# Kernel optimization log

Hardware: AMD Instinct MI355X
Metric: run time of the kernel (lower is better)

## Reference

```python
import jax, jax.numpy as jnp
import numpy as np

B, N, M, D, H, DH, DFF, L = 64, 2048, 32, 128, 4, 32, 512, 2
EPS = 1e-5


def setup_inputs() -> dict:
    key = jax.random.key(0)
    ks = jax.random.split(key, 8)
    def xav(k, shape, fan_in):
        return jax.random.normal(k, shape, jnp.float32) * (1.0 / np.sqrt(fan_in))
    return {
        "feat": jax.random.normal(ks[0], (B, N, D), jnp.float32),
        "I_pts": xav(ks[1], (L, M, D), D),                # inducing points per ISAB layer
        "Wq": xav(ks[2], (L, 2, D, H * DH), D),
        "Wk": xav(ks[3], (L, 2, D, H * DH), D),
        "Wv": xav(ks[4], (L, 2, D, H * DH), D),
        "Wo": xav(ks[5], (L, 2, H * DH, D), H * DH),
        "W1": xav(ks[6], (L, 2, D, DFF), D),
        "b1": jnp.zeros((L, 2, DFF), jnp.float32),
        "W2": xav(ks[7], (L, 2, DFF, D), DFF),
        "b2": jnp.zeros((L, 2, D), jnp.float32),
        "ln1_g": jnp.ones((L, 2, D), jnp.float32),
        "ln1_b": jnp.zeros((L, 2, D), jnp.float32),
        "ln2_g": jnp.ones((L, 2, D), jnp.float32),
        "ln2_b": jnp.zeros((L, 2, D), jnp.float32),
    }


def _layer_norm(x, g, b):
    mu = jnp.mean(x, axis=-1, keepdims=True)
    var = jnp.mean(jnp.square(x - mu), axis=-1, keepdims=True)
    return (x - mu) * jax.lax.rsqrt(var + EPS) * g + b


def _mha(q_feat, kv_feat, Wq, Wk, Wv, Wo, W1, b1, W2, b2, g1, be1, g2, be2):
    # q_feat: [B, nq, D], kv_feat: [B, nk, D]
    nq, nk = q_feat.shape[1], kv_feat.shape[1]
    Q = (q_feat @ Wq).reshape(B, nq, H, DH)
    K = (kv_feat @ Wk).reshape(B, nk, H, DH)
    V = (kv_feat @ Wv).reshape(B, nk, H, DH)
    # edge score = sum_d(q*k)/sqrt(d_head); edge_softmax normalizes over kv per query
    scores = jnp.einsum('bqhd,bkhd->bhqk', Q, K) / np.sqrt(DH)
    att = jax.nn.softmax(scores, axis=-1)
    out = jnp.einsum('bhqk,bkhd->bqhd', att, V).reshape(B, nq, H * DH)
    sa = out @ Wo
    x = _layer_norm(q_feat + sa, g1, be1)
    ffn = jax.nn.relu(x @ W1 + b1) @ W2 + b2
    return _layer_norm(x + ffn, g2, be2)


def reference(feat, I_pts, Wq, Wk, Wv, Wo, W1, b1, W2, b2, ln1_g, ln1_b, ln2_g, ln2_b):
    x = feat
    for l in range(L):  # ISAB layers
        query = jnp.broadcast_to(I_pts[l], (B, M, D))
        kv = x
        for j in range(2):  # induced -> set, then set -> induced
            rst = _mha(query, kv,
                       Wq[l, j], Wk[l, j], Wv[l, j], Wo[l, j],
                       W1[l, j], b1[l, j], W2[l, j], b2[l, j],
                       ln1_g[l, j], ln1_b[l, j], ln2_g[l, j], ln2_b[l, j])
            query, kv = kv, rst
        x = rst
    return x
```

## Files before the change

kernel.cpp:

```cpp
#include <hip/hip_runtime.h>
#include <hip/hip_bf16.h>

#define BB 64
#define NN 2048
#define MM 32
#define DD 128
#define HH 4
#define LL 2
#define BN (BB*NN)
#define BM (BB*MM)

typedef short bf16x8 __attribute__((ext_vector_type(8)));
typedef float f32x4 __attribute__((ext_vector_type(4)));
#define MFMA __builtin_amdgcn_mfma_f32_16x16x32_bf16

__device__ __forceinline__ unsigned short f2bf(float f){
  union { float f; unsigned int u; } v; v.f = f;
  unsigned int r = 0x7FFFu + ((v.u >> 16) & 1u);
  return (unsigned short)((v.u + r) >> 16);
}
__device__ __forceinline__ float bf2f(short u){
  union { unsigned int u; float f; } v; v.u = ((unsigned int)(unsigned short)u) << 16; return v.f;
}
__device__ __forceinline__ float ldf(const float* p){ return *p; }
__device__ __forceinline__ float ldf(const unsigned short* p){ return bf2f((short)*p); }
__device__ __forceinline__ void stf(float* p, float v){ *p = v; }
__device__ __forceinline__ void stf(unsigned short* p, float v){ *p = f2bf(v); }

__device__ __forceinline__ bf16x8 cvt8(const float* __restrict__ p){
  float4 a = *reinterpret_cast<const float4*>(p);
  float4 b = *reinterpret_cast<const float4*>(p + 4);
  bf16x8 r;
  r[0]=(short)f2bf(a.x); r[1]=(short)f2bf(a.y); r[2]=(short)f2bf(a.z); r[3]=(short)f2bf(a.w);
  r[4]=(short)f2bf(b.x); r[5]=(short)f2bf(b.y); r[6]=(short)f2bf(b.z); r[7]=(short)f2bf(b.w);
  return r;
}

template<int NW>
__device__ __forceinline__ void stage_img(const unsigned short* __restrict__ img,
                                          unsigned short* Wt){
  int wave = threadIdx.x >> 6, lane = threadIdx.x & 63;
  #pragma unroll
  for (int i = 0; i < 32/NW; i++){
    int off = ((i*NW + wave) << 9);
    const unsigned short* gp = img + off + lane*8;
    unsigned short* lp = Wt + off;
    __builtin_amdgcn_global_load_lds(
        (__attribute__((address_space(1))) void*)gp,
        (__attribute__((address_space(3))) void*)lp, 16, 0, 0);
  }
}

__device__ __forceinline__ bf16x8 bfrag(const unsigned short* Wt, int cb, int k0, int lane){
  int c = (cb << 4) + (lane & 15);
  int kk = (k0 + ((lane >> 4) << 3)) ^ ((c & 7) << 3);
  return *reinterpret_cast<const bf16x8*>(Wt + (c << 7) + kk);
}

__device__ __forceinline__ void load_afrag(const float* __restrict__ A, int r0, int lane,
                                           bf16x8 af[2][4]){
  int li = lane & 15, lg = lane >> 4;
  #pragma unroll
  for (int s = 0; s < 2; s++){
    const float* ap = A + (size_t)(r0 + s*16 + li) * 128 + (lg << 3);
    #pragma unroll
    for (int ks = 0; ks < 4; ks++) af[s][ks] = cvt8(ap + ks*32);
  }
}
__device__ __forceinline__ void load_afrag(const unsigned short* __restrict__ A, int r0,
                                           int lane, bf16x8 af[2][4]){
  int li = lane & 15, lg = lane >> 4;
  #pragma unroll
  for (int s = 0; s < 2; s++){
    const unsigned short* ap = A + (size_t)(r0 + s*16 + li) * 128 + (lg << 3);
    #pragma unroll
    for (int ks = 0; ks < 4; ks++) af[s][ks] = *reinterpret_cast<const bf16x8*>(ap + ks*32);
  }
}

__device__ __forceinline__ void mfma_tile32(const bf16x8 af[2][4], const unsigned short* Wt,
                                            int lane, f32x4 acc[2][8]){
  #pragma unroll
  for (int ks = 0; ks < 4; ks++){
    #pragma unroll
    for (int cb = 0; cb < 8; cb++){
      bf16x8 b = bfrag(Wt, cb, ks*32, lane);
      acc[0][cb] = MFMA(af[0][ks], b, acc[0][cb], 0, 0, 0);
      acc[1][cb] = MFMA(af[1][ks], b, acc[1][cb], 0, 0, 0);
    }
  }
}

__device__ __forceinline__ void zero_acc(f32x4 acc[2][8]){
  #pragma unroll
  for (int s = 0; s < 2; s++)
    #pragma unroll
    for (int cb = 0; cb < 8; cb++) acc[s][cb] = (f32x4){0.f,0.f,0.f,0.f};
}

__device__ __forceinline__ void store_f32(const f32x4 acc[2][8], float* __restrict__ C,
                                          int r0, int lane){
  int li = lane & 15, lg = lane >> 4;
  #pragma unroll
  for (int s = 0; s < 2; s++)
    #pragma unroll
    for (int q = 0; q < 4; q++){
      float* crow = C + (size_t)(r0 + s*16 + lg*4 + q) * 128;
      #pragma unroll
      for (int cb = 0; cb < 8; cb++) crow[cb*16 + li] = acc[s][cb][q];
    }
}
__device__ __forceinline__ void store_bf16(const f32x4 acc[2][8], unsigned short* __restrict__ C,
                                           int r0, int lane){
  int li = lane & 15, lg = lane >> 4;
  #pragma unroll
  for (int s = 0; s < 2; s++)
    #pragma unroll
    for (int q = 0; q < 4; q++){
      unsigned short* crow = C + (size_t)(r0 + s*16 + lg*4 + q) * 128;
      #pragma unroll
      for (int cb = 0; cb < 8; cb++) crow[cb*16 + li] = f2bf(acc[s][cb][q]);
    }
}
__device__ __forceinline__ void store_st2(const f32x4 acc[2][8], float* __restrict__ St2,
                                          int b, int jb, int lane){
  int li = lane & 15, lg = lane >> 4;
  #pragma unroll
  for (int s = 0; s < 2; s++)
    #pragma unroll
    for (int cb = 0; cb < 8; cb++){
      float* p = St2 + ((size_t)(b*128 + cb*16 + li))*2048 + jb + s*16 + lg*4;
      *reinterpret_cast<f32x4*>(p) = acc[s][cb];
    }
}

template<typename RT, typename OT>
__device__ __forceinline__ void ln_ep(const f32x4 acc[8], const float* __restrict__ bias,
    const RT* __restrict__ resid, unsigned int resmask,
    const float* __restrict__ g, const float* __restrict__ beta,
    OT* __restrict__ C, int r0, int lane){
  int li = lane & 15, lg = lane >> 4;
  float gv[8], bv[8], biasv[8];
  #pragma unroll
  for (int cb = 0; cb < 8; cb++){
    int col = cb*16 + li;
    gv[cb] = g[col]; bv[cb] = beta[col];
    biasv[cb] = bias ? bias[col] : 0.f;
  }
  #pragma unroll
  for (int q = 0; q < 4; q++){
    int r = r0 + lg*4 + q;
    const RT* rrow = resid + (size_t)(r & resmask) * 128;
    float v[8], sum = 0.f, ss = 0.f;
    #pragma unroll
    for (int cb = 0; cb < 8; cb++){
      float x = acc[cb][q] + biasv[cb] + ldf(rrow + cb*16 + li);
      v[cb] = x; sum += x; ss += x*x;
    }
    #pragma unroll
    for (int mk = 1; mk < 16; mk <<= 1){ sum += __shfl_xor(sum, mk); ss += __shfl_xor(ss, mk); }
    float mu = sum * (1.f/128.f);
    float var = ss * (1.f/128.f) - mu*mu;
    float rs = rsqrtf(var + 1e-5f);
    OT* crow = C + (size_t)r * 128;
    #pragma unroll
    for (int cb = 0; cb < 8; cb++)
      stf(crow + cb*16 + li, (v[cb] - mu) * rs * gv[cb] + bv[cb]);
  }
}


__global__ __launch_bounds__(256) void prep_imgs(const float* __restrict__ Wq,
    const float* __restrict__ Wk, const float* __restrict__ Wv, const float* __restrict__ Wo,
    const float* __restrict__ W1, const float* __restrict__ W2, unsigned short* __restrict__ imgs){
  int slot = blockIdx.x;
  const float* src; int ldw;
  if (slot < 16){
    int j = slot >> 2, m = slot & 3;
    const float* base = (m==0) ? Wq : (m==1) ? Wk : (m==2) ? Wv : Wo;
    src = base + j*16384; ldw = 128;
  } else if (slot < 32){
    int s = slot - 16; int j = s >> 2, dc = s & 3;
    src = W1 + j*65536 + dc*128; ldw = 512;
  } else {
    int s = slot - 32; int j = s >> 2, dc = s & 3;
    src = W2 + j*65536 + dc*16384; ldw = 128;
  }
  unsigned short* img = imgs + (size_t)slot * 16384;
  for (int i = threadIdx.x; i < 16384; i += 256){
    int k = i >> 7, c = i & 127;
    img[(c << 7) + (k ^ ((c & 7) << 3))] = f2bf(src[k*ldw + c]);
  }
}

__global__ __launch_bounds__(256) void prep_phaseA(const float* __restrict__ I,
    const float* __restrict__ Wq, const float* __restrict__ Wk, unsigned short* __restrict__ WfImg){
  __shared__ float Qi[32*128];
  for (int i = threadIdx.x; i < 4096; i += 256){
    int q = i >> 7, c = i & 127;
    float s = 0.f;
    #pragma unroll 8
    for (int d = 0; d < 128; d++) s += I[q*128 + d] * Wq[d*128 + c];
    Qi[i] = s;
  }
  __syncthreads();
  const float scale = 0.17677669529663687f;
  for (int i = threadIdx.x; i < 1024; i += 256){
    int k = (blockIdx.x << 3) + (i >> 7), c = i & 127;
    int hc = c >> 5, qc = c & 31;
    float s = 0.f;
    #pragma unroll
    for (int d = 0; d < 32; d++) s += Wk[k*128 + hc*32 + d] * Qi[qc*128 + hc*32 + d];
    WfImg[(c << 7) + (k ^ ((c & 7) << 3))] = f2bf(s * scale);
  }
}

__global__ __launch_bounds__(256) void prep_phaseB(const float* __restrict__ Wq,
    const float* __restrict__ Wo, const float* __restrict__ Khb, const float* __restrict__ Vhb,
    unsigned short* __restrict__ WfImgs, unsigned short* __restrict__ GvImgs){
  __shared__ float Ks[32*129];
  __shared__ float Vs[32*129];
  __shared__ float Wqt[128*33];
  __shared__ float Wot[128*17];
  int b = blockIdx.x >> 3, part = blockIdx.x & 7;
  int hwf = part >> 1;
  for (int i = threadIdx.x; i < 4096; i += 256){
    int k = i >> 7, c = i & 127;
    Ks[k*129 + c] = Khb[b*4096 + i];
    Vs[k*129 + c] = Vhb[b*4096 + i];
  }
  for (int i = threadIdx.x; i < 4096; i += 256){
    int ci = i >> 5, d = i & 31;
    Wqt[ci*33 + d] = Wq[ci*128 + hwf*32 + d];
  }
  for (int i = threadIdx.x; i < 2048; i += 256){
    int row = i >> 4, cl = i & 15;
    Wot[row*17 + cl] = Wo[row*128 + part*16 + cl];
  }
  __syncthreads();
  const float scale = 0.17677669529663687f;
  unsigned short* wf = WfImgs + (size_t)b*16384;
  unsigned short* gv = GvImgs + (size_t)b*16384;
  {
    int ci = threadIdx.x & 127;
    float wq[32];
    #pragma unroll
    for (int d = 0; d < 32; d++) wq[d] = Wqt[ci*33 + d];
    #pragma unroll
    for (int it = 0; it < 8; it++){
      int kp = part*16 + (threadIdx.x >> 7) + it*2;
      int k = kp & 31;
      float s = 0.f;
      #pragma unroll
      for (int d = 0; d < 32; d++) s += wq[d] * Ks[k*129 + hwf*32 + d];
      wf[(kp << 7) + (ci ^ ((kp & 7) << 3))] = f2bf(s * scale);
    }
  }
  {
    int kp = threadIdx.x & 127;
    int h = kp >> 5, k = kp & 31;
    float vv[32];
    #pragma unroll
    for (int d = 0; d < 32; d++) vv[d] = Vs[k*129 + h*32 + d];
    #pragma unroll
    for (int it = 0; it < 8; it++){
      int c = part*16 + (threadIdx.x >> 7) + it*2;
      int cl = c & 15;
      float s = 0.f;
      #pragma unroll
      for (int d = 0; d < 32; d++) s += vv[d] * Wot[(h*32 + d)*17 + cl];
      gv[(c << 7) + (kp ^ ((c & 7) << 3))] = f2bf(s);
    }
  }
}

__global__ __launch_bounds__(512) void gemm_dual(const float* __restrict__ X,
    const unsigned short* __restrict__ img0, const unsigned short* __restrict__ img1,
    float* __restrict__ St2, unsigned short* __restrict__ Vb){
  __shared__ __align__(16) unsigned short W0[16384];
  __shared__ __align__(16) unsigned short W1s[16384];
  stage_img<8>(img0, W0);
  stage_img<8>(img1, W1s);
  __syncthreads();
  int lane = threadIdx.x & 63, wave = threadIdx.x >> 6;
  int r0 = blockIdx.x*256 + wave*32;
  int b = r0 >> 11, jb = r0 & 2047;
  bf16x8 af[2][4];
  load_afrag(X, r0, lane, af);
  f32x4 acc[2][8];
  zero_acc(acc);
  mfma_tile32(af, W0, lane, acc);
  store_st2(acc, St2, b, jb, lane);
  zero_acc(acc);
  mfma_tile32(af, W1s, lane, acc);
  store_bf16(acc, Vb, r0, lane);
}

__global__ __launch_bounds__(256) void gemm_img(const float* __restrict__ A,
    const unsigned short* __restrict__ img, float* __restrict__ C){
  __shared__ __align__(16) unsigned short Wt[16384];
  stage_img<4>(img, Wt);
  __syncthreads();
  int lane = threadIdx.x & 63, wave = threadIdx.x >> 6;
  int r0 = blockIdx.x*128 + wave*32;
  bf16x8 af[2][4];
  load_afrag(A, r0, lane, af);
  f32x4 acc[2][8];
  zero_acc(acc);
  mfma_tile32(af, Wt, lane, acc);
  store_f32(acc, C, r0, lane);
}

__global__ __launch_bounds__(256) void gemm_ln_f32A(const float* __restrict__ A,
    const unsigned short* __restrict__ img, const float* __restrict__ resid, unsigned int resmask,
    const float* __restrict__ g, const float* __restrict__ beta, float* __restrict__ C){
  __shared__ __align__(16) unsigned short Wt[16384];
  stage_img<4>(img, Wt);
  __syncthreads();
  int lane = threadIdx.x & 63, wave = threadIdx.x >> 6;
  int r0 = blockIdx.x*128 + wave*32;
  bf16x8 af[2][4];
  load_afrag(A, r0, lane, af);
  f32x4 acc[2][8];
  zero_acc(acc);
  mfma_tile32(af, Wt, lane, acc);
  ln_ep(acc[0], nullptr, resid, resmask, g, beta, C, r0,      lane);
  ln_ep(acc[1], nullptr, resid, resmask, g, beta, C, r0 + 16, lane);
}

__global__ __launch_bounds__(512) void attn_pv(const float* __restrict__ St2,
    const unsigned short* __restrict__ V, float* __restrict__ O){
  __shared__ __align__(16) unsigned short Vt[2][4096];
  __shared__ __align__(16) float Ocomb[4][64][4];
  __shared__ float scomb[4][16];
  int b = blockIdx.x >> 2, h = blockIdx.x & 3;
  int lane = threadIdx.x & 63, w = threadIdx.x >> 6;
  int li = lane & 15, lg = lane >> 4;
  int qh = w & 1, dh = (w >> 1) & 1, jh = w >> 2;
  int tq = w & 3;
  const float* Sp = St2 + ((size_t)(b*128 + h*32 + qh*16 + li)) * 2048 + jh*1024;
  const unsigned short* Vb = V + (size_t)b*NN*128 + h*32;
  unsigned short* VtJ = Vt[jh];
  int vrow = tq*32 + (lane >> 2);
  int vd0  = (lane & 3) * 8;
  const unsigned short* vsrc = Vb + ((size_t)(jh*1024 + vrow))*128 + vd0;

  f32x4 acc = (f32x4){0.f,0.f,0.f,0.f};
  float s = 0.f;
  f32x4 Ar[2][4][2];
  bf16x8 vr[2][2];

  #pragma unroll
  for (int t = 0; t < 2; t++)
    vr[0][t] = *reinterpret_cast<const bf16x8*>(vsrc + (size_t)t*16*128);
  #pragma unroll
  for (int ks = 0; ks < 4; ks++){
    Ar[0][ks][0] = *reinterpret_cast<const f32x4*>(Sp + ks*32 + lg*8);
    Ar[0][ks][1] = *reinterpret_cast<const f32x4*>(Sp + ks*32 + lg*8 + 4);
  }

  #pragma unroll
  for (int c = 0; c < 8; c++){
    const int cur = c & 1, nxt = cur ^ 1;
    __syncthreads();
    #pragma unroll
    for (int t = 0; t < 2; t++){
      int jl = vrow + t*16;
      #pragma unroll
      for (int e = 0; e < 8; e++){
        int d = vd0 + e;
        VtJ[(d << 7) + (jl ^ ((d & 7) << 3))] = (unsigned short)vr[cur][t][e];
      }
    }
    __syncthreads();
    if (c < 7){
      #pragma unroll
      for (int t = 0; t < 2; t++)
        vr[nxt][t] = *reinterpret_cast<const bf16x8*>(vsrc + ((size_t)(c+1)*128 + t*16)*128);
      #pragma unroll
      for (int ks = 0; ks < 4; ks++){
        Ar[nxt][ks][0] = *reinterpret_cast<const f32x4*>(Sp + (c+1)*128 + ks*32 + lg*8);
        Ar[nxt][ks][1] = *reinterpret_cast<const f32x4*>(Sp + (c+1)*128 + ks*32 + lg*8 + 4);
      }
    }
    #pragma unroll
    for (int ks = 0; ks < 4; ks++){
      bf16x8 a;
      #pragma unroll
      for (int i = 0; i < 4; i++){
        float pv = __expf(fminf(Ar[cur][ks][0][i], 60.f));
        s += pv; a[i] = (short)f2bf(pv);
      }
      #pragma unroll
      for (int i = 0; i < 4; i++){
        float pv = __expf(fminf(Ar[cur][ks][1][i], 60.f));
        s += pv; a[4+i] = (short)f2bf(pv);
      }
      bf16x8 bb = bfrag(VtJ, dh, ks*32, lane);
      acc = MFMA(a, bb, acc, 0, 0, 0);
    }
  }
  s += __shfl_xor(s, 16);
  s += __shfl_xor(s, 32);
  if (jh == 1){
    *reinterpret_cast<f32x4*>(&Ocomb[tq][lane][0]) = acc;
    if (lg == 0) scomb[tq][li] = s;
  }
  __syncthreads();
  if (jh == 0){
    acc += *reinterpret_cast<const f32x4*>(&Ocomb[tq][lane][0]);
    float inv = 1.f / (s + scomb[tq][li]);
    float* op = O + ((size_t)(b*MM + qh*16))*128 + h*32 + dh*16 + li;
    #pragma unroll
    for (int r = 0; r < 4; r++){
      float iv = __shfl(inv, lg*4 + r);
      op[(size_t)(lg*4 + r)*128] = acc[r] * iv;
    }
  }
}

__global__ __launch_bounds__(512) void attn_fused(const float* __restrict__ X,
    const unsigned short* __restrict__ WfImgs, const unsigned short* __restrict__ GvImgs,
    const float* __restrict__ g, const float* __restrict__ beta,
    unsigned short* __restrict__ X1){
  extern __shared__ __align__(16) unsigned short sm[];
  unsigned short* ht  = sm;
  unsigned short* WtF = sm + 32768;
  unsigned short* WtG = sm + 49152;
  int b = blockIdx.x >> 3;
  stage_img<8>(WfImgs + (size_t)b*16384, WtF);
  stage_img<8>(GvImgs + (size_t)b*16384, WtG);
  int lane = threadIdx.x & 63, wave = threadIdx.x >> 6;
  int li = lane & 15, lg = lane >> 4;
  int r0 = blockIdx.x*256 + wave*32;
  bf16x8 af[2][4];
  load_afrag(X, r0, lane, af);
  f32x4 acc[2][8];
  zero_acc(acc);
  __syncthreads();
  mfma_tile32(af, WtF, lane, acc);
  #pragma unroll
  for (int s = 0; s < 2; s++){
    #pragma unroll
    for (int q = 0; q < 4; q++){
      int rl = wave*32 + s*16 + lg*4 + q;
      #pragma unroll
      for (int h = 0; h < 4; h++){
        float v0 = acc[s][2*h][q], v1 = acc[s][2*h+1][q];
        float m = fmaxf(v0, v1);
        #pragma unroll
        for (int mk = 1; mk < 16; mk <<= 1) m = fmaxf(m, __shfl_xor(m, mk));
        float p0 = __expf(v0 - m), p1 = __expf(v1 - m);
        float ss = p0 + p1;
        #pragma unroll
        for (int mk = 1; mk < 16; mk <<= 1) ss += __shfl_xor(ss, mk);
        float inv = 1.f / ss;
        int c0 = h*32 + li, c1 = h*32 + 16 + li;
        ht[(rl << 7) + (c0 ^ ((rl & 7) << 3))] = f2bf(p0 * inv);
        ht[(rl << 7) + (c1 ^ ((rl & 7) << 3))] = f2bf(p1 * inv);
      }
    }
  }
  __syncthreads();
  zero_acc(acc);
  #pragma unroll
  for (int ks = 0; ks < 4; ks++){
    bf16x8 a[2];
    #pragma unroll
    for (int s = 0; s < 2; s++){
      int rl = wave*32 + s*16 + li;
      int kk = (ks*32 + (lg << 3)) ^ ((rl & 7) << 3);
      a[s] = *reinterpret_cast<const bf16x8*>(ht + (rl << 7) + kk);
    }
    #pragma unroll
    for (int cb = 0; cb < 8; cb++){
      bf16x8 bb = bfrag(WtG, cb, ks*32, lane);
      acc[0][cb] = MFMA(a[0], bb, acc[0][cb], 0, 0, 0);
      acc[1][cb] = MFMA(a[1], bb, acc[1][cb], 0, 0, 0);
    }
  }
  ln_ep(acc[0], nullptr, X, 0xFFFFFFFFu, g, beta, X1, r0,      lane);
  ln_ep(acc[1], nullptr, X, 0xFFFFFFFFu, g, beta, X1, r0 + 16, lane);
}

template<typename TA>
__global__ __launch_bounds__(512) void ffn_big(const TA* __restrict__ X,
    const unsigned short* __restrict__ W1i, const float* __restrict__ b1,
    const unsigned short* __restrict__ W2i, const float* __restrict__ b2,
    const float* __restrict__ g, const float* __restrict__ beta,
    float* __restrict__ OUT){
  extern __shared__ __align__(16) unsigned short sm[];
  unsigned short* ht  = sm;
  unsigned short* Wt0 = sm + 32768;
  unsigned short* Wt1 = sm + 49152;
  int lane = threadIdx.x & 63, wave = threadIdx.x >> 6;
  int li = lane & 15, lg = lane >> 4;
  int r0 = blockIdx.x*256 + wave*32;
  bf16x8 af[2][4];
  load_afrag(X, r0, lane, af);
  f32x4 accO[2][8];
  zero_acc(accO);
  stage_img<8>(W1i, Wt0);
  stage_img<8>(W2i, Wt1);
  __syncthreads();
  for (int dc = 0; dc < 4; dc++){
    if (dc > 0) stage_img<8>(W2i + dc*16384, Wt1);
    f32x4 acc1[2][8];
    zero_acc(acc1);
    mfma_tile32(af, Wt0, lane, acc1);
    #pragma unroll
    for (int s = 0; s < 2; s++)
      #pragma unroll
      for (int q = 0; q < 4; q++){
        int rl = wave*32 + s*16 + lg*4 + q;
        #pragma unroll
        for (int cb = 0; cb < 8; cb++){
          int col = cb*16 + li;
          float v = acc1[s][cb][q] + b1[dc*128 + col];
          v = fmaxf(v, 0.f);
          ht[(rl << 7) + (col ^ ((rl & 7) << 3))] = f2bf(v);
        }
      }
    __syncthreads();
    if (dc < 3) stage_img<8>(W1i + (dc+1)*16384, Wt0);
    #pragma unroll
    for (int ks = 0; ks < 4; ks++){
      bf16x8 a[2];
      #pragma unroll
      for (int s = 0; s < 2; s++){
        int rl = wave*32 + s*16 + li;
        int kk = (ks*32 + (lg << 3)) ^ ((rl & 7) << 3);
        a[s] = *reinterpret_cast<const bf16x8*>(ht + (rl << 7) + kk);
      }
      #pragma unroll
      for (int cb = 0; cb < 8; cb++){
        bf16x8 bb = bfrag(Wt1, cb, ks*32, lane);
        accO[0][cb] = MFMA(a[0], bb, accO[0][cb], 0, 0, 0);
        accO[1][cb] = MFMA(a[1], bb, accO[1][cb], 0, 0, 0);
      }
    }
    __syncthreads();
  }
  ln_ep(accO[0], b2, X, 0xFFFFFFFFu, g, beta, OUT, r0,      lane);
  ln_ep(accO[1], b2, X, 0xFFFFFFFFu, g, beta, OUT, r0 + 16, lane);
}

extern "C" void kernel_launch(void* const* d_in, const int* in_sizes, int n_in,
                              void* d_out, int out_size, void* d_ws, size_t ws_size,
                              hipStream_t stream){
  (void)in_sizes; (void)n_in; (void)out_size; (void)ws_size;
  const float* feat = (const float*)d_in[0];
  const float* Ipts = (const float*)d_in[1];
  const float* Wq   = (const float*)d_in[2];
  const float* Wk   = (const float*)d_in[3];
  const float* Wv   = (const float*)d_in[4];
  const float* Wo   = (const float*)d_in[5];
  const float* W1   = (const float*)d_in[6];
  const float* b1   = (const float*)d_in[7];
  const float* W2   = (const float*)d_in[8];
  const float* b2   = (const float*)d_in[9];
  const float* g1   = (const float*)d_in[10];
  const float* be1  = (const float*)d_in[11];
  const float* g2   = (const float*)d_in[12];
  const float* be2  = (const float*)d_in[13];
  float* out = (float*)d_out;

  float* bigA = (float*)d_ws;
  unsigned short* bigX1 = (unsigned short*)bigA;
  unsigned short* bigV = (unsigned short*)(bigA + (size_t)BN*128);
  float* Oind  = (float*)(bigV + (size_t)BN*128);
  float* x1ind = Oind  + (size_t)BM*128;
  float* Hind  = x1ind + (size_t)BM*128;
  float* Khb   = Hind  + (size_t)BM*128;
  float* Vhb   = Khb   + (size_t)BM*128;
  unsigned short* imgs = (unsigned short*)(Vhb + (size_t)BM*128);

  unsigned short* imgQKVO = imgs;
  unsigned short* imgW1   = imgs + (size_t)16*16384;
  unsigned short* imgW2   = imgs + (size_t)32*16384;
  unsigned short* imgWf   = imgs + (size_t)48*16384;
  unsigned short* wfB     = imgs + (size_t)50*16384;
  unsigned short* gvB     = imgs + (size_t)114*16384;

  prep_imgs<<<48, 256, 0, stream>>>(Wq, Wk, Wv, Wo, W1, W2, imgs);

  for (int l = 0; l < LL; l++){
    const float* x = (l == 0) ? feat : out;
    const float* Il = Ipts + l*MM*DD;
    int j0 = l*2, j1 = l*2 + 1;
    prep_phaseA<<<16, 256, 0, stream>>>(Il, Wq + j0*16384, Wk + j0*16384, imgWf + l*16384);
    gemm_dual<<<BN/256, 512, 0, stream>>>(x, imgWf + l*16384, imgQKVO + (j0*4+2)*16384,
                                          bigA, bigV);
    attn_pv<<<BB*HH, 512, 0, stream>>>(bigA, bigV, Oind);
    gemm_ln_f32A<<<BM/128, 256, 0, stream>>>(Oind, imgQKVO + (j0*4+3)*16384, Il, 31u,
                                             g1 + j0*128, be1 + j0*128, x1ind);
    ffn_big<float><<<BM/256, 512, 131072, stream>>>(x1ind, imgW1 + (size_t)j0*4*16384, b1 + j0*512,
                                        imgW2 + (size_t)j0*4*16384, b2 + j0*128,
                                        g2 + j0*128, be2 + j0*128, Hind);
    gemm_img<<<BM/128, 256, 0, stream>>>(Hind, imgQKVO + (j1*4+1)*16384, Khb);
    gemm_img<<<BM/128, 256, 0, stream>>>(Hind, imgQKVO + (j1*4+2)*16384, Vhb);
    prep_phaseB<<<BB*8, 256, 0, stream>>>(Wq + j1*16384, Wo + j1*16384, Khb, Vhb, wfB, gvB);
    attn_fused<<<BN/256, 512, 131072, stream>>>(x, wfB, gvB,
                                                g1 + j1*128, be1 + j1*128, bigX1);
    ffn_big<unsigned short><<<BN/256, 512, 131072, stream>>>(bigX1, imgW1 + (size_t)j1*4*16384, b1 + j1*512,
                                        imgW2 + (size_t)j1*4*16384, b2 + j1*128,
                                        g2 + j1*128, be2 + j1*128, out);
  }
}
```

Baseline: 658.0 us.

## Swap MFMA operand order to keep intermediates in registers via lane shuffles

Result: faster. 569.0 us (-13.5%).

```diff
diff --git a/kernel.cpp b/kernel.cpp
--- a/kernel.cpp
+++ b/kernel.cpp
@@ -12,20 +12,35 @@
 
 typedef short bf16x8 __attribute__((ext_vector_type(8)));
 typedef float f32x4 __attribute__((ext_vector_type(4)));
+typedef unsigned int u32;
 #define MFMA __builtin_amdgcn_mfma_f32_16x16x32_bf16
 
 __device__ __forceinline__ unsigned short f2bf(float f){
-  union { float f; unsigned int u; } v; v.f = f;
-  unsigned int r = 0x7FFFu + ((v.u >> 16) & 1u);
+  union { float f; u32 u; } v; v.f = f;
+  u32 r = 0x7FFFu + ((v.u >> 16) & 1u);
   return (unsigned short)((v.u + r) >> 16);
 }
-__device__ __forceinline__ float bf2f(short u){
-  union { unsigned int u; float f; } v; v.u = ((unsigned int)(unsigned short)u) << 16; return v.f;
+__device__ __forceinline__ float bf2f(unsigned short u){
+  union { u32 u; float f; } v; v.u = ((u32)u) << 16; return v.f;
+}
+__device__ __forceinline__ u32 pack2(float a, float b){
+  return (u32)f2bf(a) | ((u32)f2bf(b) << 16);
 }
 __device__ __forceinline__ float ldf(const float* p){ return *p; }
-__device__ __forceinline__ float ldf(const unsigned short* p){ return bf2f((short)*p); }
+__device__ __forceinline__ float ldf(const unsigned short* p){ return bf2f(*p); }
 __device__ __forceinline__ void stf(float* p, float v){ *p = v; }
 __device__ __forceinline__ void stf(unsigned short* p, float v){ *p = f2bf(v); }
+
+__device__ __forceinline__ f32x4 ld4(const float* p){ return *reinterpret_cast<const f32x4*>(p); }
+__device__ __forceinline__ f32x4 ld4(const unsigned short* p){
+  ushort4 u = *reinterpret_cast<const ushort4*>(p);
+  f32x4 r; r[0]=bf2f(u.x); r[1]=bf2f(u.y); r[2]=bf2f(u.z); r[3]=bf2f(u.w); return r;
+}
+__device__ __forceinline__ void st4(float* p, f32x4 v){ *reinterpret_cast<f32x4*>(p) = v; }
+__device__ __forceinline__ void st4(unsigned short* p, f32x4 v){
+  ushort4 u; u.x=f2bf(v[0]); u.y=f2bf(v[1]); u.z=f2bf(v[2]); u.w=f2bf(v[3]);
+  *reinterpret_cast<ushort4*>(p) = u;
+}
 
 __device__ __forceinline__ bf16x8 cvt8(const float* __restrict__ p){
   float4 a = *reinterpret_cast<const float4*>(p);
@@ -90,6 +105,18 @@
     }
   }
 }
+__device__ __forceinline__ void mfma_swp(const bf16x8 af[2][4], const unsigned short* Wt,
+                                         int lane, f32x4 acc[2][8]){
+  #pragma unroll
+  for (int ks = 0; ks < 4; ks++){
+    #pragma unroll
+    for (int cb = 0; cb < 8; cb++){
+      bf16x8 w = bfrag(Wt, cb, ks*32, lane);
+      acc[0][cb] = MFMA(w, af[0][ks], acc[0][cb], 0, 0, 0);
+      acc[1][cb] = MFMA(w, af[1][ks], acc[1][cb], 0, 0, 0);
+    }
+  }
+}
 
 __device__ __forceinline__ void zero_acc(f32x4 acc[2][8]){
   #pragma unroll
@@ -167,6 +194,64 @@
     for (int cb = 0; cb < 8; cb++)
       stf(crow + cb*16 + li, (v[cb] - mu) * rs * gv[cb] + bv[cb]);
   }
+}
+
+template<typename RT, typename OT>
+__device__ __forceinline__ void ln_swp(const f32x4 accO[2][8], const float* __restrict__ bias,
+    const RT* __restrict__ resid, const float* __restrict__ g, const float* __restrict__ beta,
+    OT* __restrict__ C, int r0, int lane){
+  int li = lane & 15, lg = lane >> 4;
+  #pragma unroll
+  for (int s = 0; s < 2; s++){
+    int r = r0 + s*16 + li;
+    const RT* rr = resid + (size_t)r * 128;
+    float v[8][4]; float sum = 0.f, ss = 0.f;
+    #pragma unroll
+    for (int cb = 0; cb < 8; cb++){
+      int c0 = cb*16 + lg*4;
+      f32x4 rq = ld4(rr + c0);
+      f32x4 bq = bias ? *reinterpret_cast<const f32x4*>(bias + c0) : (f32x4){0.f,0.f,0.f,0.f};
+      #pragma unroll
+      for (int q = 0; q < 4; q++){
+        float x = accO[s][cb][q] + bq[q] + rq[q];
+        v[cb][q] = x; sum += x; ss += x*x;
+      }
+    }
+    sum += __shfl_xor(sum, 16); ss += __shfl_xor(ss, 16);
+    sum += __shfl_xor(sum, 32); ss += __shfl_xor(ss, 32);
+    float mu = sum * (1.f/128.f);
+    float var = ss * (1.f/128.f) - mu*mu;
+    float rs = rsqrtf(var + 1e-5f);
+    OT* co = C + (size_t)r * 128;
+    #pragma unroll
+    for (int cb = 0; cb < 8; cb++){
+      int c0 = cb*16 + lg*4;
+      f32x4 gq = *reinterpret_cast<const f32x4*>(g + c0);
+      f32x4 tq = *reinterpret_cast<const f32x4*>(beta + c0);
+      f32x4 o;
+      #pragma unroll
+      for (int q = 0; q < 4; q++) o[q] = (v[cb][q] - mu) * rs * gq[q] + tq[q];
+      st4(co + c0, o);
+    }
+  }
+}
+
+__device__ __forceinline__ bf16x8 redist(const u32 pk[2][8][2], int s, int ks,
+                                         int t, int srcA, int srcB){
+  u32 a0 = (u32)__shfl((int)pk[s][2*ks][0],   srcA);
+  u32 a1 = (u32)__shfl((int)pk[s][2*ks+1][0], srcA);
+  u32 a2 = (u32)__shfl((int)pk[s][2*ks][1],   srcA);
+  u32 a3 = (u32)__shfl((int)pk[s][2*ks+1][1], srcA);
+  u32 b0 = (u32)__shfl((int)pk[s][2*ks][0],   srcB);
+  u32 b1 = (u32)__shfl((int)pk[s][2*ks+1][0], srcB);
+  u32 b2 = (u32)__shfl((int)pk[s][2*ks][1],   srcB);
+  u32 b3 = (u32)__shfl((int)pk[s][2*ks+1][1], srcB);
+  union { u32 u[4]; bf16x8 v; } r;
+  r.u[0] = t ? a1 : a0;
+  r.u[1] = t ? a3 : a2;
+  r.u[2] = t ? b1 : b0;
+  r.u[3] = t ? b3 : b2;
+  return r.v;
 }
 
 
@@ -274,7 +359,8 @@
   }
 }
 
-__global__ __launch_bounds__(512) void gemm_dual(const float* __restrict__ X,
+template<typename TX>
+__global__ __launch_bounds__(512) void gemm_dual(const TX* __restrict__ X,
     const unsigned short* __restrict__ img0, const unsigned short* __restrict__ img1,
     float* __restrict__ St2, unsigned short* __restrict__ Vb){
   __shared__ __align__(16) unsigned short W0[16384];
@@ -419,136 +505,128 @@
   }
 }
 
-__global__ __launch_bounds__(512) void attn_fused(const float* __restrict__ X,
+template<typename TX>
+__global__ __launch_bounds__(256, 2) void attn_swp(const TX* __restrict__ X,
     const unsigned short* __restrict__ WfImgs, const unsigned short* __restrict__ GvImgs,
     const float* __restrict__ g, const float* __restrict__ beta,
     unsigned short* __restrict__ X1){
-  extern __shared__ __align__(16) unsigned short sm[];
-  unsigned short* ht  = sm;
-  unsigned short* WtF = sm + 32768;
-  unsigned short* WtG = sm + 49152;
-  int b = blockIdx.x >> 3;
-  stage_img<8>(WfImgs + (size_t)b*16384, WtF);
-  stage_img<8>(GvImgs + (size_t)b*16384, WtG);
+  __shared__ __align__(16) unsigned short WtF[16384];
+  __shared__ __align__(16) unsigned short WtG[16384];
+  int b = blockIdx.x >> 4;
+  stage_img<4>(WfImgs + (size_t)b*16384, WtF);
+  stage_img<4>(GvImgs + (size_t)b*16384, WtG);
   int lane = threadIdx.x & 63, wave = threadIdx.x >> 6;
   int li = lane & 15, lg = lane >> 4;
-  int r0 = blockIdx.x*256 + wave*32;
+  int r0 = blockIdx.x*128 + wave*32;
   bf16x8 af[2][4];
   load_afrag(X, r0, lane, af);
-  f32x4 acc[2][8];
-  zero_acc(acc);
   __syncthreads();
-  mfma_tile32(af, WtF, lane, acc);
-  #pragma unroll
-  for (int s = 0; s < 2; s++){
-    #pragma unroll
-    for (int q = 0; q < 4; q++){
-      int rl = wave*32 + s*16 + lg*4 + q;
-      #pragma unroll
-      for (int h = 0; h < 4; h++){
-        float v0 = acc[s][2*h][q], v1 = acc[s][2*h+1][q];
-        float m = fmaxf(v0, v1);
-        #pragma unroll
-        for (int mk = 1; mk < 16; mk <<= 1) m = fmaxf(m, __shfl_xor(m, mk));
-        float p0 = __expf(v0 - m), p1 = __expf(v1 - m);
-        float ss = p0 + p1;
-        #pragma unroll
-        for (int mk = 1; mk < 16; mk <<= 1) ss += __shfl_xor(ss, mk);
-        float inv = 1.f / ss;
-        int c0 = h*32 + li, c1 = h*32 + 16 + li;
-        ht[(rl << 7) + (c0 ^ ((rl & 7) << 3))] = f2bf(p0 * inv);
-        ht[(rl << 7) + (c1 ^ ((rl & 7) << 3))] = f2bf(p1 * inv);
-      }
-    }
-  }
-  __syncthreads();
-  zero_acc(acc);
+  f32x4 sv[2][8];
+  zero_acc(sv);
+  mfma_swp(af, WtF, lane, sv);
+  u32 pk[2][8][2];
+  #pragma unroll
+  for (int s = 0; s < 2; s++)
+    #pragma unroll
+    for (int h = 0; h < 4; h++){
+      float p[8];
+      #pragma unroll
+      for (int q = 0; q < 4; q++){ p[q] = sv[s][2*h][q]; p[4+q] = sv[s][2*h+1][q]; }
+      float m = fmaxf(fmaxf(fmaxf(p[0],p[1]),fmaxf(p[2],p[3])),
+                      fmaxf(fmaxf(p[4],p[5]),fmaxf(p[6],p[7])));
+      m = fmaxf(m, __shfl_xor(m, 16));
+      m = fmaxf(m, __shfl_xor(m, 32));
+      float sm = 0.f;
+      #pragma unroll
+      for (int i = 0; i < 8; i++){ p[i] = __expf(p[i] - m); sm += p[i]; }
+      sm += __shfl_xor(sm, 16);
+      sm += __shfl_xor(sm, 32);
+      float inv = 1.f / sm;
+      pk[s][2*h][0]   = pack2(p[0]*inv, p[1]*inv);
+      pk[s][2*h][1]   = pack2(p[2]*inv, p[3]*inv);
+      pk[s][2*h+1][0] = pack2(p[4]*inv, p[5]*inv);
+      pk[s][2*h+1][1] = pack2(p[6]*inv, p[7]*inv);
+    }
+  int t = lg >> 1;
+  int srcA = li + (((lane >> 4) & 1) << 5);
+  int srcB = srcA + 16;
+  f32x4 accO[2][8];
+  zero_acc(accO);
   #pragma unroll
   for (int ks = 0; ks < 4; ks++){
-    bf16x8 a[2];
-    #pragma unroll
-    for (int s = 0; s < 2; s++){
-      int rl = wave*32 + s*16 + li;
-      int kk = (ks*32 + (lg << 3)) ^ ((rl & 7) << 3);
-      a[s] = *reinterpret_cast<const bf16x8*>(ht + (rl << 7) + kk);
-    }
+    bf16x8 hb0 = redist(pk, 0, ks, t, srcA, srcB);
+    bf16x8 hb1 = redist(pk, 1, ks, t, srcA, srcB);
     #pragma unroll
     for (int cb = 0; cb < 8; cb++){
-      bf16x8 bb = bfrag(WtG, cb, ks*32, lane);
-      acc[0][cb] = MFMA(a[0], bb, acc[0][cb], 0, 0, 0);
-      acc[1][cb] = MFMA(a[1], bb, acc[1][cb], 0, 0, 0);
-    }
-  }
-  ln_ep(acc[0], nullptr, X, 0xFFFFFFFFu, g, beta, X1, r0,      lane);
-  ln_ep(acc[1], nullptr, X, 0xFFFFFFFFu, g, beta, X1, r0 + 16, lane);
-}
-
-template<typename TA>
-__global__ __launch_bounds__(512) void ffn_big(const TA* __restrict__ X,
+      bf16x8 w = bfrag(WtG, cb, ks*32, lane);
+      accO[0][cb] = MFMA(w, hb0, accO[0][cb], 0, 0, 0);
+      accO[1][cb] = MFMA(w, hb1, accO[1][cb], 0, 0, 0);
+    }
+  }
+  ln_swp(accO, nullptr, X, g, beta, X1, r0, lane);
+}
+
+template<typename TA, typename TO>
+__global__ __launch_bounds__(256, 2) void ffn_swp(const TA* __restrict__ X,
     const unsigned short* __restrict__ W1i, const float* __restrict__ b1,
     const unsigned short* __restrict__ W2i, const float* __restrict__ b2,
     const float* __restrict__ g, const float* __restrict__ beta,
-    float* __restrict__ OUT){
-  extern __shared__ __align__(16) unsigned short sm[];
-  unsigned short* ht  = sm;
-  unsigned short* Wt0 = sm + 32768;
-  unsigned short* Wt1 = sm + 49152;
+    TO* __restrict__ OUT){
+  __shared__ __align__(16) unsigned short Wt0[16384];
+  __shared__ __align__(16) unsigned short Wt1[16384];
   int lane = threadIdx.x & 63, wave = threadIdx.x >> 6;
   int li = lane & 15, lg = lane >> 4;
-  int r0 = blockIdx.x*256 + wave*32;
+  int r0 = blockIdx.x*128 + wave*32;
   bf16x8 af[2][4];
   load_afrag(X, r0, lane, af);
   f32x4 accO[2][8];
   zero_acc(accO);
-  stage_img<8>(W1i, Wt0);
-  stage_img<8>(W2i, Wt1);
+  stage_img<4>(W1i, Wt0);
+  stage_img<4>(W2i, Wt1);
   __syncthreads();
+  int t = lg >> 1;
+  int srcA = li + (((lane >> 4) & 1) << 5);
+  int srcB = srcA + 16;
   for (int dc = 0; dc < 4; dc++){
-    if (dc > 0) stage_img<8>(W2i + dc*16384, Wt1);
     f32x4 acc1[2][8];
     zero_acc(acc1);
-    mfma_tile32(af, Wt0, lane, acc1);
+    mfma_swp(af, Wt0, lane, acc1);
+    u32 pk[2][8][2];
     #pragma unroll
     for (int s = 0; s < 2; s++)
       #pragma unroll
-      for (int q = 0; q < 4; q++){
-        int rl = wave*32 + s*16 + lg*4 + q;
-        #pragma unroll
-        for (int cb = 0; cb < 8; cb++){
-          int col = cb*16 + li;
-          float v = acc1[s][cb][q] + b1[dc*128 + col];
-          v = fmaxf(v, 0.f);
-          ht[(rl << 7) + (col ^ ((rl & 7) << 3))] = f2bf(v);
-        }
+      for (int cb = 0; cb < 8; cb++){
+        f32x4 bq = *reinterpret_cast<const f32x4*>(b1 + dc*128 + cb*16 + lg*4);
+        float v0 = fmaxf(acc1[s][cb][0] + bq[0], 0.f);
+        float v1 = fmaxf(acc1[s][cb][1] + bq[1], 0.f);
+        float v2 = fmaxf(acc1[s][cb][2] + bq[2], 0.f);
+        float v3 = fmaxf(acc1[s][cb][3] + bq[3], 0.f);
+        pk[s][cb][0] = pack2(v0, v1);
+        pk[s][cb][1] = pack2(v2, v3);
       }
     __syncthreads();
-    if (dc < 3) stage_img<8>(W1i + (dc+1)*16384, Wt0);
+    if (dc < 3) stage_img<4>(W1i + (dc+1)*16384, Wt0);
     #pragma unroll
     for (int ks = 0; ks < 4; ks++){
-      bf16x8 a[2];
-      #pragma unroll
-      for (int s = 0; s < 2; s++){
-        int rl = wave*32 + s*16 + li;
-        int kk = (ks*32 + (lg << 3)) ^ ((rl & 7) << 3);
-        a[s] = *reinterpret_cast<const bf16x8*>(ht + (rl << 7) + kk);
+      bf16x8 hb0 = redist(pk, 0, ks, t, srcA, srcB);
+      bf16x8 hb1 = redist(pk, 1, ks, t, srcA, srcB);
+      #pragma unroll
+      for (int cb = 0; cb < 8; cb++){
+        bf16x8 w = bfrag(Wt1, cb, ks*32, lane);
+        accO[0][cb] = MFMA(w, hb0, accO[0][cb], 0, 0, 0);
+        accO[1][cb] = MFMA(w, hb1, accO[1][cb], 0, 0, 0);
       }
-      #pragma unroll
-      for (int cb = 0; cb < 8; cb++){
-        bf16x8 bb = bfrag(Wt1, cb, ks*32, lane);
-        accO[0][cb] = MFMA(a[0], bb, accO[0][cb], 0, 0, 0);
-        accO[1][cb] = MFMA(a[1], bb, accO[1][cb], 0, 0, 0);
-      }
     }
     __syncthreads();
-  }
-  ln_ep(accO[0], b2, X, 0xFFFFFFFFu, g, beta, OUT, r0,      lane);
-  ln_ep(accO[1], b2, X, 0xFFFFFFFFu, g, beta, OUT, r0 + 16, lane);
+    if (dc < 3) stage_img<4>(W2i + (dc+1)*16384, Wt1);
+  }
+  ln_swp(accO, b2, X, g, beta, OUT, r0, lane);
 }
 
 extern "C" void kernel_launch(void* const* d_in, const int* in_sizes, int n_in,
                               void* d_out, int out_size, void* d_ws, size_t ws_size,
                               hipStream_t stream){
-  (void)in_sizes; (void)n_in; (void)out_size; (void)ws_size;
+  (void)in_sizes; (void)n_in; (void)out_size;
   const float* feat = (const float*)d_in[0];
   const float* Ipts = (const float*)d_in[1];
   const float* Wq   = (const float*)d_in[2];
@@ -581,29 +659,46 @@
   unsigned short* imgWf   = imgs + (size_t)48*16384;
   unsigned short* wfB     = imgs + (size_t)50*16384;
   unsigned short* gvB     = imgs + (size_t)114*16384;
+  unsigned short* xb      = imgs + (size_t)178*16384;
+  size_t need = (size_t)((char*)(xb + (size_t)BN*128) - (char*)d_ws);
+  bool useXb = (ws_size >= need);
 
   prep_imgs<<<48, 256, 0, stream>>>(Wq, Wk, Wv, Wo, W1, W2, imgs);
 
   for (int l = 0; l < LL; l++){
-    const float* x = (l == 0) ? feat : out;
+    const float* xf = (l == 0) ? feat : out;
+    bool xBf = (l > 0) && useXb;
     const float* Il = Ipts + l*MM*DD;
     int j0 = l*2, j1 = l*2 + 1;
     prep_phaseA<<<16, 256, 0, stream>>>(Il, Wq + j0*16384, Wk + j0*16384, imgWf + l*16384);
-    gemm_dual<<<BN/256, 512, 0, stream>>>(x, imgWf + l*16384, imgQKVO + (j0*4+2)*16384,
-                                          bigA, bigV);
+    if (xBf)
+      gemm_dual<unsigned short><<<BN/256, 512, 0, stream>>>(xb, imgWf + l*16384,
+          imgQKVO + (j0*4+2)*16384, bigA, bigV);
+    else
+      gemm_dual<float><<<BN/256, 512, 0, stream>>>(xf, imgWf + l*16384,
+          imgQKVO + (j0*4+2)*16384, bigA, bigV);
     attn_pv<<<BB*HH, 512, 0, stream>>>(bigA, bigV, Oind);
     gemm_ln_f32A<<<BM/128, 256, 0, stream>>>(Oind, imgQKVO + (j0*4+3)*16384, Il, 31u,
                                              g1 + j0*128, be1 + j0*128, x1ind);
-    ffn_big<float><<<BM/256, 512, 131072, stream>>>(x1ind, imgW1 + (size_t)j0*4*16384, b1 + j0*512,
-                                        imgW2 + (size_t)j0*4*16384, b2 + j0*128,
-                                        g2 + j0*128, be2 + j0*128, Hind);
+    ffn_swp<float, float><<<BM/128, 256, 0, stream>>>(x1ind, imgW1 + (size_t)j0*4*16384,
+        b1 + j0*512, imgW2 + (size_t)j0*4*16384, b2 + j0*128,
+        g2 + j0*128, be2 + j0*128, Hind);
     gemm_img<<<BM/128, 256, 0, stream>>>(Hind, imgQKVO + (j1*4+1)*16384, Khb);
     gemm_img<<<BM/128, 256, 0, stream>>>(Hind, imgQKVO + (j1*4+2)*16384, Vhb);
     prep_phaseB<<<BB*8, 256, 0, stream>>>(Wq + j1*16384, Wo + j1*16384, Khb, Vhb, wfB, gvB);
-    attn_fused<<<BN/256, 512, 131072, stream>>>(x, wfB, gvB,
-                                                g1 + j1*128, be1 + j1*128, bigX1);
-    ffn_big<unsigned short><<<BN/256, 512, 131072, stream>>>(bigX1, imgW1 + (size_t)j1*4*16384, b1 + j1*512,
-                                        imgW2 + (size_t)j1*4*16384, b2 + j1*128,
-                                        g2 + j1*128, be2 + j1*128, out);
-  }
-}
+    if (xBf)
+      attn_swp<unsigned short><<<BN/128, 256, 0, stream>>>(xb, wfB, gvB,
+          g1 + j1*128, be1 + j1*128, bigX1);
+    else
+      attn_swp<float><<<BN/128, 256, 0, stream>>>(xf, wfB, gvB,
+          g1 + j1*128, be1 + j1*128, bigX1);
+    if (l == 0 && useXb)
+      ffn_swp<unsigned short, unsigned short><<<BN/128, 256, 0, stream>>>(bigX1,
+          imgW1 + (size_t)j1*4*16384, b1 + j1*512, imgW2 + (size_t)j1*4*16384, b2 + j1*128,
+          g2 + j1*128, be2 + j1*128, xb);
+    else
+      ffn_swp<unsigned short, float><<<BN/128, 256, 0, stream>>>(bigX1,
+          imgW1 + (size_t)j1*4*16384, b1 + j1*512, imgW2 + (size_t)j1*4*16384, b2 + j1*128,
+          g2 + j1*128, be2 + j1*128, out);
+  }
+}
```
